# Optimization experiments

Hardware: AMD Instinct MI355X
Metric: run time of the kernel (lower is better)

The kernel has to match this reference:

```python
import jax, jax.numpy as jnp
import numpy as np
from jax import lax

N_PCD, N_RGB = 5000, 15000
C_PCD, C_RGB = 32, 128
N_ANCHOR, SA_RADIUS, SA_NS = 4096, 0.1, 32
NB_RADIUS, NB_K = 0.2, 64


def _fps(xyz, npoint):
    # farthest point sampling, first index = 0 (CUDA convention)
    n = xyz.shape[0]
    def step(carry, _):
        dists, last = carry
        d = jnp.sum((xyz - xyz[last]) ** 2, axis=-1)
        dists = jnp.minimum(dists, d)
        nxt = jnp.argmax(dists).astype(jnp.int32)
        return (dists, nxt), nxt
    init = (jnp.full((n,), 1e10, xyz.dtype), jnp.int32(0))
    _, rest = lax.scan(step, init, None, length=npoint - 1)
    return jnp.concatenate([jnp.zeros((1,), jnp.int32), rest])


def _ball_query(radius, nsample, points, centers):
    # first `nsample` points within radius of each center; pad with first hit
    n = points.shape[0]
    d2 = jnp.sum((centers[:, None, :] - points[None, :, :]) ** 2, axis=-1)  # [M,N]
    key_ = jnp.where(d2 < radius * radius, jnp.arange(n, dtype=jnp.float32), float(n))
    vals, idx = lax.top_k(-key_, nsample)  # smallest in-range indices first
    valid = vals > -(float(n) - 0.5)
    return jnp.where(valid, idx, idx[:, :1])


def _detection_scores(xyz, features):
    # xyz [N,3], features [N,C]
    n = xyz.shape[0]
    nb = _ball_query(NB_RADIUS, NB_K, xyz, xyz)                       # [N,K]
    feats = jnp.concatenate([features, jnp.zeros_like(features[:1])], 0)
    nb = jnp.concatenate([nb, jnp.full((1, NB_K), n, nb.dtype)], 0)   # shadow row
    feats = feats / (jnp.max(feats) + 1e-6)
    nf = feats[nb]                                                    # [N+1,K,C]
    num = jnp.maximum(jnp.sum((nb >= 0).astype(feats.dtype), 1, keepdims=True), 1.0)
    mean = jnp.sum(nf, axis=1) / num
    local_max = jax.nn.softplus(feats - mean)
    dw_max = jnp.max(feats, axis=1, keepdims=True)
    dw_score = feats / (1e-6 + dw_max)
    return jnp.max(local_max * dw_score, axis=1)[:-1]                 # [N]


def setup_inputs() -> dict:
    key = jax.random.key(0)
    ks = jax.random.split(key, 12)
    def w(k, o, i):
        return jax.random.normal(k, (o, i), jnp.float32) * 0.05
    return {
        'pcd_xyz': jax.random.uniform(ks[0], (N_PCD, 3), jnp.float32),
        'pcd_features': jax.random.normal(ks[1], (N_PCD, C_PCD), jnp.float32),
        'rgb_xyz': jax.random.uniform(ks[2], (1, N_RGB, 3), jnp.float32),
        'rgb_features': jax.random.normal(ks[3], (1, C_RGB, N_RGB), jnp.float32),
        'sa_W1': w(ks[4], 128, 3 + C_PCD + C_RGB), 'sa_b1': jnp.zeros((128,), jnp.float32),
        'sa_W2': w(ks[5], 128, 128), 'sa_b2': jnp.zeros((128,), jnp.float32),
        'sa_W3': w(ks[6], 128, 128), 'sa_b3': jnp.zeros((128,), jnp.float32),
        'fp_W1': w(ks[7], 128, C_PCD + C_RGB + 128), 'fp_b1': jnp.zeros((128,), jnp.float32),
        'fp_W2': w(ks[8], 32, 128), 'fp_b2': jnp.zeros((32,), jnp.float32),
    }


def reference(pcd_xyz, pcd_features, rgb_xyz, rgb_features,
              sa_W1, sa_b1, sa_W2, sa_b2, sa_W3, sa_b3,
              fp_W1, fp_b1, fp_W2, fp_b2):
    rgb_xyz = rgb_xyz[0]                       # [N_rgb,3]
    rgb_feat = rgb_features[0].T               # [N_rgb,128]
    # zero-padded modality channels, then concat clouds
    pcd_exp = jnp.concatenate([pcd_features, jnp.zeros((N_PCD, C_RGB), pcd_features.dtype)], 1)
    rgb_exp = jnp.concatenate([jnp.zeros((N_RGB, C_PCD), rgb_feat.dtype), rgb_feat], 1)
    xyz = jnp.concatenate([pcd_xyz, rgb_xyz], 0)      # [N,3]
    feat = jnp.concatenate([pcd_exp, rgb_exp], 0)     # [N,160]

    # --- PointnetSAModuleVotes: FPS + ball query + shared MLP + max pool ---
    fidx = _fps(xyz, N_ANCHOR)
    new_xyz = xyz[fidx]                               # [A,3]
    nb = _ball_query(SA_RADIUS, SA_NS, xyz, new_xyz)  # [A,S]
    gxyz = (xyz[nb] - new_xyz[:, None, :]) / SA_RADIUS  # normalize_xyz
    g = jnp.concatenate([gxyz, feat[nb]], -1)          # [A,S,163]
    h = g
    for W, b in ((sa_W1, sa_b1), (sa_W2, sa_b2), (sa_W3, sa_b3)):
        h = jax.nn.relu(jnp.einsum('asc,oc->aso', h, W) + b)
    sa_feat = jnp.max(h, axis=1)                       # [A,128]

    # --- PointnetFPModule: three-NN inverse-distance interpolation + MLP ---
    d2 = jnp.sum((xyz[:, None, :] - new_xyz[None, :, :]) ** 2, -1)  # [N,A]
    negd, nn_idx = lax.top_k(-d2, 3)
    wgt = 1.0 / (-negd + 1e-8)
    wgt = wgt / jnp.sum(wgt, -1, keepdims=True)
    interp = jnp.einsum('nkc,nk->nc', sa_feat[nn_idx], wgt)         # [N,128]
    f = jnp.concatenate([interp, feat], -1)                         # [N,288]
    f = jax.nn.relu(f @ fp_W1.T + fp_b1)
    f = jax.nn.relu(f @ fp_W2.T + fp_b2)                            # [N,32]

    fp_feat = f[:N_PCD]                                             # [N_pcd,32]
    vote_scores = _detection_scores(pcd_xyz, fp_feat)               # [N_pcd]
    norm = jnp.maximum(jnp.linalg.norm(fp_feat, axis=1, keepdims=True), 1e-12)
    vote_features = fp_feat / norm
    return (pcd_xyz, vote_scores, vote_features)
```

## Files before the change

kernel.cpp:

```cpp
#include <hip/hip_runtime.h>

#define N_ALL 20000
#define NPCD  5000
#define NRGB  15000
#define CPCD  32
#define CRGB  128
#define CF    160
#define NA    4096
#define SANS  32
#define NBK   64
#define K1    163
#define K1P   168
#define HD    128
#define FPK   288
#define NSOA  20480

__global__ void prep_kernel(const float* __restrict__ pcd_xyz,
                            const float* __restrict__ pcd_feat,
                            const float* __restrict__ rgb_xyz,
                            const float* __restrict__ rgb_feat,
                            const float* __restrict__ sa_W1,
                            float* __restrict__ xyz,
                            float* __restrict__ feat,
                            float* __restrict__ W1p) {
  const int TOT = N_ALL*CF + N_ALL*3 + HD*K1P;
  for (int id = blockIdx.x*blockDim.x + threadIdx.x; id < TOT; id += gridDim.x*blockDim.x) {
    if (id < N_ALL*CF) {
      int r = id / CF, c = id - r*CF;
      float v = 0.0f;
      if (r < NPCD) { if (c < CPCD) v = pcd_feat[r*CPCD + c]; }
      else          { if (c >= CPCD) v = rgb_feat[(c - CPCD)*NRGB + (r - NPCD)]; }
      feat[id] = v;
    } else if (id < N_ALL*CF + N_ALL*3) {
      int e = id - N_ALL*CF;
      xyz[e] = (e < NPCD*3) ? pcd_xyz[e] : rgb_xyz[e - NPCD*3];
    } else {
      int e = id - (N_ALL*CF + N_ALL*3);
      int o = e / K1P, c = e - o*K1P;
      W1p[e] = (c < K1) ? sa_W1[o*K1 + c] : 0.0f;
    }
  }
}

static __device__ __forceinline__ unsigned spread4(unsigned v) {
  return (v & 1u) | ((v & 2u) << 2) | ((v & 4u) << 4) | ((v & 8u) << 6);
}
static __device__ __forceinline__ unsigned morton12(float x, float y, float z) {
  int ix = (int)(x * 16.0f); ix = ix < 0 ? 0 : (ix > 15 ? 15 : ix);
  int iy = (int)(y * 16.0f); iy = iy < 0 ? 0 : (iy > 15 ? 15 : iy);
  int iz = (int)(z * 16.0f); iz = iz < 0 ? 0 : (iz > 15 ? 15 : iz);
  return spread4((unsigned)ix) | (spread4((unsigned)iy) << 1) | (spread4((unsigned)iz) << 2);
}

__global__ void __launch_bounds__(1024) sort_kernel(const float* __restrict__ pcd_xyz,
                                                    const float* __restrict__ rgb_xyz,
                                                    float* __restrict__ xsoa,
                                                    float* __restrict__ ysoa,
                                                    float* __restrict__ zsoa,
                                                    unsigned short* __restrict__ orig16) {
  __shared__ unsigned hist[4096];
  __shared__ unsigned ssum[1024];
  const int t = threadIdx.x;
  for (int i = t; i < 4096; i += 1024) hist[i] = 0u;
  __syncthreads();
  for (int p = t; p < N_ALL; p += 1024) {
    float x, y, z;
    if (p < NPCD) { x = pcd_xyz[3*p]; y = pcd_xyz[3*p+1]; z = pcd_xyz[3*p+2]; }
    else { int q = p - NPCD; x = rgb_xyz[3*q]; y = rgb_xyz[3*q+1]; z = rgb_xyz[3*q+2]; }
    atomicAdd(&hist[morton12(x, y, z)], 1u);
  }
  __syncthreads();
  unsigned h0 = hist[4*t], h1 = hist[4*t+1], h2 = hist[4*t+2], h3 = hist[4*t+3];
  unsigned mysum = h0 + h1 + h2 + h3;
  ssum[t] = mysum;
  __syncthreads();
  for (int off = 1; off < 1024; off <<= 1) {
    unsigned add = (t >= off) ? ssum[t - off] : 0u;
    __syncthreads();
    ssum[t] += add;
    __syncthreads();
  }
  unsigned excl = ssum[t] - mysum;
  hist[4*t]   = excl;
  hist[4*t+1] = excl + h0;
  hist[4*t+2] = excl + h0 + h1;
  hist[4*t+3] = excl + h0 + h1 + h2;
  __syncthreads();
  for (int p = t; p < N_ALL; p += 1024) {
    float x, y, z;
    if (p < NPCD) { x = pcd_xyz[3*p]; y = pcd_xyz[3*p+1]; z = pcd_xyz[3*p+2]; }
    else { int q = p - NPCD; x = rgb_xyz[3*q]; y = rgb_xyz[3*q+1]; z = rgb_xyz[3*q+2]; }
    unsigned dst = atomicAdd(&hist[morton12(x, y, z)], 1u);
    xsoa[dst] = x; ysoa[dst] = y; zsoa[dst] = z; orig16[dst] = (unsigned short)p;
  }
  for (int i = N_ALL + t; i < NSOA; i += 1024) {
    xsoa[i] = 0.0f; ysoa[i] = 0.0f; zsoa[i] = 0.0f; orig16[i] = 0;
  }
}

typedef float v2f __attribute__((ext_vector_type(2)));

template <int CTRL>
static __device__ __forceinline__ unsigned dpp_min_u32(unsigned v) {
  int s = __builtin_amdgcn_update_dpp((int)v, (int)v, CTRL, 0xF, 0xF, false);
  unsigned u = (unsigned)s;
  return v < u ? v : u;
}

__global__ void __launch_bounds__(1024)
__attribute__((amdgpu_waves_per_eu(2, 4)))
fps_kernel(const float* __restrict__ xsoa,
           const float* __restrict__ ysoa,
           const float* __restrict__ zsoa,
           const unsigned short* __restrict__ orig16,
           const float* __restrict__ pcd_xyz,
           int* __restrict__ fidx,
           float* __restrict__ axyz) {
  #pragma clang fp contract(off)
  const int t = threadIdx.x;
  const int lane = t & 63;
  __shared__ unsigned long long ls[4];
  if (t < 4) ls[t] = ~0ull;
  const int base = 20 * t;
  v2f X[10], Y[10], Z[10], D[10];
  unsigned idk[20];
  #pragma unroll
  for (int j = 0; j < 10; j++) {
    int p = base + 2*j;
    X[j] = *(const v2f*)(xsoa + p);
    Y[j] = *(const v2f*)(ysoa + p);
    Z[j] = *(const v2f*)(zsoa + p);
    D[j].x = (p     < N_ALL) ? 1e10f : -1.0f;
    D[j].y = (p + 1 < N_ALL) ? 1e10f : -1.0f;
    idk[2*j]   = ((unsigned)orig16[p]     << 15) | (unsigned)p;
    idk[2*j+1] = ((unsigned)orig16[p + 1] << 15) | (unsigned)(p + 1);
  }
  float blx = 1e30f, bhx = -1e30f, bly = 1e30f, bhy = -1e30f, blz = 1e30f, bhz = -1e30f;
  #pragma unroll
  for (int j = 0; j < 10; j++) {
    blx = fminf(blx, fminf(X[j].x, X[j].y)); bhx = fmaxf(bhx, fmaxf(X[j].x, X[j].y));
    bly = fminf(bly, fminf(Y[j].x, Y[j].y)); bhy = fmaxf(bhy, fmaxf(Y[j].x, Y[j].y));
    blz = fminf(blz, fminf(Z[j].x, Z[j].y)); bhz = fmaxf(bhz, fmaxf(Z[j].x, Z[j].y));
  }
  float tmaxc = (base < N_ALL) ? 1e10f : -1.0f;
  unsigned invd = 0xFFFFFFFFu, k32 = 0xFFFFFFFFu;
  float cx = pcd_xyz[0], cy = pcd_xyz[1], cz = pcd_xyz[2];
  if (t == 0) { fidx[0] = 0; axyz[0] = cx; axyz[1] = cy; axyz[2] = cz; }
  __syncthreads();
  for (int it = 1; it < NA; ++it) {
    const int s = it & 3;
    float tdx = fmaxf(fmaxf(blx - cx, cx - bhx), 0.0f);
    float tdy = fmaxf(fmaxf(bly - cy, cy - bhy), 0.0f);
    float tdz = fmaxf(fmaxf(blz - cz, cz - bhz), 0.0f);
    float lb2 = (tdx*tdx + tdy*tdy) + tdz*tdz;
    if (lb2 * 0.99f < tmaxc) {
      v2f cxv = {cx, cx}, cyv = {cy, cy}, czv = {cz, cz};
      float m[10];
      #pragma unroll
      for (int j = 0; j < 10; j++) {
        v2f dx = X[j] - cxv;
        v2f dy = Y[j] - cyv;
        v2f dz = Z[j] - czv;
        v2f d  = (dx*dx + dy*dy) + dz*dz;
        D[j].x = fminf(D[j].x, d.x);
        D[j].y = fminf(D[j].y, d.y);
        m[j] = fmaxf(D[j].x, D[j].y);
      }
      float m0 = fmaxf(m[0], m[1]), m1 = fmaxf(m[2], m[3]);
      float m2 = fmaxf(m[4], m[5]), m3 = fmaxf(m[6], m[7]);
      float tmax = fmaxf(fmaxf(fmaxf(m0, m1), fmaxf(m2, m3)), fmaxf(m[8], m[9]));
      tmaxc = tmax;
      invd = ~__float_as_uint(tmax);
      unsigned kk = 0xFFFFFFFFu;
      #pragma unroll
      for (int j = 0; j < 10; j++) {
        unsigned c0 = (D[j].x == tmax) ? idk[2*j]     : 0xFFFFFFFFu;
        unsigned c1 = (D[j].y == tmax) ? idk[2*j + 1] : 0xFFFFFFFFu;
        unsigned cm = c0 < c1 ? c0 : c1;
        kk = kk < cm ? kk : cm;
      }
      k32 = kk;
    }
    unsigned wi = invd;
    wi = dpp_min_u32<0x111>(wi);
    wi = dpp_min_u32<0x112>(wi);
    wi = dpp_min_u32<0x114>(wi);
    wi = dpp_min_u32<0x118>(wi);
    wi = dpp_min_u32<0x142>(wi);
    wi = dpp_min_u32<0x143>(wi);
    unsigned wmin = (unsigned)__builtin_amdgcn_readlane((int)wi, 63);
    unsigned sel = (invd == wmin) ? k32 : 0xFFFFFFFFu;
    sel = dpp_min_u32<0x111>(sel);
    sel = dpp_min_u32<0x112>(sel);
    sel = dpp_min_u32<0x114>(sel);
    sel = dpp_min_u32<0x118>(sel);
    sel = dpp_min_u32<0x142>(sel);
    sel = dpp_min_u32<0x143>(sel);
    if (lane == 63)
      atomicMin(&ls[s], ((unsigned long long)wmin << 32) | (unsigned long long)sel);
    if (t == 0) ls[(it + 2) & 3] = ~0ull;
    __syncthreads();
    unsigned lo = (unsigned)ls[s];
    unsigned pos = lo & 32767u;
    cx = xsoa[pos]; cy = ysoa[pos]; cz = zsoa[pos];
    if (t == 0) {
      fidx[it] = (int)(lo >> 15);
      axyz[3*it] = cx; axyz[3*it+1] = cy; axyz[3*it+2] = cz;
    }
  }
}

__global__ void sa_bq_kernel(const float* __restrict__ xyz,
                             const float* __restrict__ axyz,
                             int* __restrict__ nb) {
  #pragma clang fp contract(off)
  int wv = threadIdx.x >> 6, lane = threadIdx.x & 63;
  int a = blockIdx.x*4 + wv;
  float ax = axyz[3*a], ay = axyz[3*a+1], az = axyz[3*a+2];
  int cnt = 0, my = 0;
  for (int base = 0; base < N_ALL; base += 64) {
    int p = base + lane;
    bool in = false;
    if (p < N_ALL) {
      float dx = ax - xyz[3*p], dy = ay - xyz[3*p+1], dz = az - xyz[3*p+2];
      float d2 = (dx*dx + dy*dy) + dz*dz;
      in = d2 < 0.01f;
    }
    unsigned long long mask = __ballot(in);
    while (mask && cnt < SANS) {
      int b = __builtin_ctzll(mask);
      mask &= mask - 1;
      if (cnt == lane) my = base + b;
      cnt++;
    }
    if (cnt >= SANS) break;
  }
  int f0 = __shfl(my, 0);
  if (lane < SANS) nb[a*SANS + lane] = (lane < cnt) ? my : f0;
}

__global__ void det_bq_kernel(const float* __restrict__ pxyz,
                              int* __restrict__ nb) {
  #pragma clang fp contract(off)
  int wv = threadIdx.x >> 6, lane = threadIdx.x & 63;
  int i = blockIdx.x*4 + wv;
  float ax = pxyz[3*i], ay = pxyz[3*i+1], az = pxyz[3*i+2];
  int cnt = 0, my = 0;
  for (int base = 0; base < NPCD; base += 64) {
    int p = base + lane;
    bool in = false;
    if (p < NPCD) {
      float dx = ax - pxyz[3*p], dy = ay - pxyz[3*p+1], dz = az - pxyz[3*p+2];
      float d2 = (dx*dx + dy*dy) + dz*dz;
      in = d2 < 0.04f;
    }
    unsigned long long mask = __ballot(in);
    while (mask && cnt < NBK) {
      int b = __builtin_ctzll(mask);
      mask &= mask - 1;
      if (cnt == lane) my = base + b;
      cnt++;
    }
    if (cnt >= NBK) break;
  }
  int f0 = __shfl(my, 0);
  nb[i*NBK + lane] = (lane < cnt) ? my : f0;
}

__global__ void __launch_bounds__(128) sa_mlp_kernel(const float* __restrict__ xyz,
                                                     const float* __restrict__ feat,
                                                     const float* __restrict__ axyz,
                                                     const int* __restrict__ nb,
                                                     const float* __restrict__ W1p,
                                                     const float* __restrict__ b1,
                                                     const float* __restrict__ W2,
                                                     const float* __restrict__ b2,
                                                     const float* __restrict__ W3,
                                                     const float* __restrict__ b3,
                                                     float* __restrict__ sa_feat) {
  __shared__ float g[SANS*K1P];
  __shared__ float h1[SANS*HD];
  __shared__ int nbs[SANS];
  int a = blockIdx.x, tid = threadIdx.x;
  if (tid < SANS) nbs[tid] = nb[a*SANS + tid];
  float ax = axyz[3*a], ay = axyz[3*a+1], az = axyz[3*a+2];
  __syncthreads();
  for (int e = tid; e < SANS*K1P; e += 128) {
    int s = e / K1P, c = e - s*K1P;
    float v = 0.0f;
    int p = nbs[s];
    if (c < 3) {
      float pc  = xyz[3*p + c];
      float acx = (c == 0) ? ax : ((c == 1) ? ay : az);
      v = (pc - acx) / 0.1f;
    } else if (c < K1) {
      v = feat[p*CF + (c - 3)];
    }
    g[e] = v;
  }
  __syncthreads();
  const int o = tid;
  float acc[SANS];
  #pragma unroll
  for (int s = 0; s < SANS; s++) acc[s] = b1[o];
  for (int kc = 0; kc < 21; kc++) {
    const float4* wp = (const float4*)(W1p + o*K1P + kc*8);
    float4 w0 = wp[0], w1 = wp[1];
    #pragma unroll
    for (int s = 0; s < SANS; s++) {
      const float4* gp = (const float4*)(g + s*K1P + kc*8);
      float4 g0 = gp[0], g1 = gp[1];
      acc[s] += w0.x*g0.x + w0.y*g0.y + w0.z*g0.z + w0.w*g0.w
              + w1.x*g1.x + w1.y*g1.y + w1.z*g1.z + w1.w*g1.w;
    }
  }
  #pragma unroll
  for (int s = 0; s < SANS; s++) h1[s*HD + o] = fmaxf(acc[s], 0.0f);
  __syncthreads();
  #pragma unroll
  for (int s = 0; s < SANS; s++) acc[s] = b2[o];
  for (int kc = 0; kc < 16; kc++) {
    const float4* wp = (const float4*)(W2 + o*HD + kc*8);
    float4 w0 = wp[0], w1 = wp[1];
    #pragma unroll
    for (int s = 0; s < SANS; s++) {
      const float4* gp = (const float4*)(h1 + s*HD + kc*8);
      float4 g0 = gp[0], g1 = gp[1];
      acc[s] += w0.x*g0.x + w0.y*g0.y + w0.z*g0.z + w0.w*g0.w
              + w1.x*g1.x + w1.y*g1.y + w1.z*g1.z + w1.w*g1.w;
    }
  }
  float* h2 = g;
  #pragma unroll
  for (int s = 0; s < SANS; s++) h2[s*HD + o] = fmaxf(acc[s], 0.0f);
  __syncthreads();
  #pragma unroll
  for (int s = 0; s < SANS; s++) acc[s] = b3[o];
  for (int kc = 0; kc < 16; kc++) {
    const float4* wp = (const float4*)(W3 + o*HD + kc*8);
    float4 w0 = wp[0], w1 = wp[1];
    #pragma unroll
    for (int s = 0; s < SANS; s++) {
      const float4* gp = (const float4*)(h2 + s*HD + kc*8);
      float4 g0 = gp[0], g1 = gp[1];
      acc[s] += w0.x*g0.x + w0.y*g0.y + w0.z*g0.z + w0.w*g0.w
              + w1.x*g1.x + w1.y*g1.y + w1.z*g1.z + w1.w*g1.w;
    }
  }
  float m = 0.0f;
  #pragma unroll
  for (int s = 0; s < SANS; s++) m = fmaxf(m, fmaxf(acc[s], 0.0f));
  sa_feat[a*HD + o] = m;
}

#define INSERT3(v) { if ((v) < t0){ t2=t1; t1=t0; t0=(v);} \
                     else if ((v) < t1){ t2=t1; t1=(v);} \
                     else if ((v) < t2){ t2=(v);} }

__global__ void nn_interp_kernel(const float* __restrict__ xyz,
                                 const float* __restrict__ feat,
                                 const float* __restrict__ axyz,
                                 const float* __restrict__ sa_feat,
                                 float* __restrict__ F) {
  #pragma clang fp contract(off)
  int wv = threadIdx.x >> 6, lane = threadIdx.x & 63;
  int p = blockIdx.x*4 + wv;
  float px = xyz[3*p], py = xyz[3*p+1], pz = xyz[3*p+2];
  unsigned long long t0 = ~0ull, t1 = ~0ull, t2 = ~0ull;
  for (int j = 0; j < 64; j++) {
    int a = lane + (j << 6);
    float dx = px - axyz[3*a], dy = py - axyz[3*a+1], dz = pz - axyz[3*a+2];
    float d2 = (dx*dx + dy*dy) + dz*dz;
    unsigned long long pk = ((unsigned long long)__float_as_uint(d2) << 32) | (unsigned)a;
    INSERT3(pk);
  }
  #pragma unroll
  for (int off = 1; off < 64; off <<= 1) {
    unsigned long long b0 = __shfl_xor(t0, off);
    unsigned long long b1 = __shfl_xor(t1, off);
    unsigned long long b2 = __shfl_xor(t2, off);
    INSERT3(b0); INSERT3(b1); INSERT3(b2);
  }
  float d0 = __uint_as_float((unsigned)(t0 >> 32));
  float d1 = __uint_as_float((unsigned)(t1 >> 32));
  float d2v = __uint_as_float((unsigned)(t2 >> 32));
  int a0 = (int)(t0 & 0xFFFFFFFFull), a1 = (int)(t1 & 0xFFFFFFFFull), a2 = (int)(t2 & 0xFFFFFFFFull);
  float w0 = 1.0f/(d0 + 1e-8f), w1 = 1.0f/(d1 + 1e-8f), w2 = 1.0f/(d2v + 1e-8f);
  float wsum = w0 + w1 + w2;
  w0 /= wsum; w1 /= wsum; w2 /= wsum;
  const float* s0 = sa_feat + a0*HD;
  const float* s1 = sa_feat + a1*HD;
  const float* s2 = sa_feat + a2*HD;
  float* Fr = F + p*FPK;
  Fr[lane]      = w0*s0[lane]    + w1*s1[lane]    + w2*s2[lane];
  Fr[lane + 64] = w0*s0[lane+64] + w1*s1[lane+64] + w2*s2[lane+64];
  const float* fr = feat + p*CF;
  Fr[HD + lane]      = fr[lane];
  Fr[HD + lane + 64] = fr[lane + 64];
  if (lane < 32) Fr[HD + 128 + lane] = fr[128 + lane];
}

__global__ void __launch_bounds__(128) fp1_kernel(const float* __restrict__ F,
                                                  const float* __restrict__ W,
                                                  const float* __restrict__ b,
                                                  float* __restrict__ H) {
  __shared__ float A[32*FPK];
  int base = blockIdx.x*32, tid = threadIdx.x;
  for (int e = tid; e < 32*FPK; e += 128) {
    int r = e / FPK; int gr = base + r;
    A[e] = (gr < NPCD) ? F[gr*FPK + (e - r*FPK)] : 0.0f;
  }
  __syncthreads();
  const int o = tid;
  float acc[32];
  #pragma unroll
  for (int r = 0; r < 32; r++) acc[r] = b[o];
  for (int kc = 0; kc < 36; kc++) {
    const float4* wp = (const float4*)(W + o*FPK + kc*8);
    float4 w0 = wp[0], w1 = wp[1];
    #pragma unroll
    for (int r = 0; r < 32; r++) {
      const float4* ap = (const float4*)(A + r*FPK + kc*8);
      float4 a0 = ap[0], a1 = ap[1];
      acc[r] += w0.x*a0.x + w0.y*a0.y + w0.z*a0.z + w0.w*a0.w
              + w1.x*a1.x + w1.y*a1.y + w1.z*a1.z + w1.w*a1.w;
    }
  }
  #pragma unroll
  for (int r = 0; r < 32; r++) {
    int gr = base + r;
    if (gr < NPCD) H[gr*HD + o] = fmaxf(acc[r], 0.0f);
  }
}

__global__ void __launch_bounds__(256) fp2_kernel(const float* __restrict__ Hin,
                                                  const float* __restrict__ W,
                                                  const float* __restrict__ b,
                                                  float* __restrict__ fpf,
                                                  unsigned* __restrict__ gmax) {
  if (blockIdx.x == 0 && threadIdx.x == 0) *gmax = 0u;
  __shared__ float A[32*HD];
  int base = blockIdx.x*32, tid = threadIdx.x;
  for (int e = tid; e < 32*HD; e += 256) {
    int r = e >> 7; int gr = base + r;
    A[e] = (gr < NPCD) ? Hin[gr*HD + (e & 127)] : 0.0f;
  }
  __syncthreads();
  int o = tid & 31, rg = tid >> 5;
  float acc[4];
  #pragma unroll
  for (int j = 0; j < 4; j++) acc[j] = b[o];
  for (int kc = 0; kc < 16; kc++) {
    const float4* wp = (const float4*)(W + o*HD + kc*8);
    float4 w0 = wp[0], w1 = wp[1];
    #pragma unroll
    for (int j = 0; j < 4; j++) {
      int r = rg + (j << 3);
      const float4* ap = (const float4*)(A + r*HD + kc*8);
      float4 a0 = ap[0], a1 = ap[1];
      acc[j] += w0.x*a0.x + w0.y*a0.y + w0.z*a0.z + w0.w*a0.w
              + w1.x*a1.x + w1.y*a1.y + w1.z*a1.z + w1.w*a1.w;
    }
  }
  #pragma unroll
  for (int j = 0; j < 4; j++) {
    int gr = base + rg + (j << 3);
    if (gr < NPCD) fpf[gr*CPCD + o] = fmaxf(acc[j], 0.0f);
  }
}

__global__ void gmax_kernel(const float* __restrict__ fpf, unsigned* __restrict__ gmax) {
  int id = blockIdx.x*256 + threadIdx.x;
  float m = (id < NPCD*CPCD) ? fpf[id] : 0.0f;
  #pragma unroll
  for (int off = 1; off < 64; off <<= 1) m = fmaxf(m, __shfl_xor(m, off));
  if ((threadIdx.x & 63) == 0) atomicMax(gmax, __float_as_uint(m));
}

__global__ void det_score_kernel(const float* __restrict__ fpf,
                                 const int* __restrict__ nbd,
                                 const unsigned* __restrict__ gmax,
                                 float* __restrict__ outs) {
  int wv = threadIdx.x >> 6, lane = threadIdx.x & 63;
  int i = blockIdx.x*4 + wv;
  float g = __uint_as_float(*gmax);
  float scale = 1.0f / (g + 1e-6f);
  int c = lane & 31, h = lane >> 5;
  float sum = 0.0f;
  const int* nbr = nbd + i*NBK + h*32;
  for (int k = 0; k < 32; k++) {
    int idx = nbr[k];
    sum += fpf[idx*CPCD + c];
  }
  sum += __shfl_xor(sum, 32);
  float mean = (sum * scale) * 0.015625f;
  float fi = fpf[i*CPCD + c] * scale;
  float x = fi - mean;
  float lm = fmaxf(x, 0.0f) + log1pf(expf(-fabsf(x)));
  float dm = fi;
  #pragma unroll
  for (int off = 1; off < 64; off <<= 1) dm = fmaxf(dm, __shfl_xor(dm, off));
  float dw = fi / (1e-6f + dm);
  float pr = lm * dw;
  #pragma unroll
  for (int off = 1; off < 64; off <<= 1) pr = fmaxf(pr, __shfl_xor(pr, off));
  if (lane == 0) outs[i] = pr;
}

__global__ void vote_out_kernel(const float* __restrict__ pcd_xyz,
                                const float* __restrict__ fpf,
                                float* __restrict__ dout) {
  int id = blockIdx.x*256 + threadIdx.x;
  if (id < NPCD*3) dout[id] = pcd_xyz[id];
  int r = id - NPCD*3;
  if (r >= 0 && r < NPCD) {
    float ss = 0.0f;
    const float* fr = fpf + r*CPCD;
    #pragma unroll
    for (int cc = 0; cc < CPCD; cc++) ss += fr[cc]*fr[cc];
    float nrm = fmaxf(sqrtf(ss), 1e-12f);
    float* vf = dout + NPCD*3 + NPCD + r*CPCD;
    #pragma unroll
    for (int cc = 0; cc < CPCD; cc++) vf[cc] = fr[cc] / nrm;
  }
}

extern "C" void kernel_launch(void* const* d_in, const int* in_sizes, int n_in,
                              void* d_out, int out_size, void* d_ws, size_t ws_size,
                              hipStream_t stream) {
  const float* pcd_xyz      = (const float*)d_in[0];
  const float* pcd_features = (const float*)d_in[1];
  const float* rgb_xyz      = (const float*)d_in[2];
  const float* rgb_features = (const float*)d_in[3];
  const float* sa_W1 = (const float*)d_in[4];
  const float* sa_b1 = (const float*)d_in[5];
  const float* sa_W2 = (const float*)d_in[6];
  const float* sa_b2 = (const float*)d_in[7];
  const float* sa_W3 = (const float*)d_in[8];
  const float* sa_b3 = (const float*)d_in[9];
  const float* fp_W1 = (const float*)d_in[10];
  const float* fp_b1 = (const float*)d_in[11];
  const float* fp_W2 = (const float*)d_in[12];
  const float* fp_b2 = (const float*)d_in[13];
  float* out = (float*)d_out;

  float* xyz  = (float*)d_ws;
  float* feat = xyz  + 60000;
  float* W1p  = feat + 3200000;
  float* axyz = W1p  + 21504;
  float* saf  = axyz + 12288;
  float* F    = saf  + 524288;
  float* Hb   = F    + 1440000;
  float* fpf  = Hb   + 640000;
  int*   fidx = (int*)(fpf + 160000);
  int*   nbsa = fidx + 4096;
  int*   nbdet= nbsa + 131072;
  unsigned* gmaxp = (unsigned*)(nbdet + 320000);
  float* xsoa = (float*)(gmaxp + 1);
  float* ysoa = xsoa + NSOA;
  float* zsoa = ysoa + NSOA;
  unsigned short* orig16 = (unsigned short*)(zsoa + NSOA);

  prep_kernel<<<2048, 256, 0, stream>>>(pcd_xyz, pcd_features, rgb_xyz, rgb_features,
                                        sa_W1, xyz, feat, W1p);
  sort_kernel<<<1, 1024, 0, stream>>>(pcd_xyz, rgb_xyz, xsoa, ysoa, zsoa, orig16);
  fps_kernel<<<1, 1024, 0, stream>>>(xsoa, ysoa, zsoa, orig16, pcd_xyz, fidx, axyz);
  sa_bq_kernel<<<1024, 256, 0, stream>>>(xyz, axyz, nbsa);
  sa_mlp_kernel<<<4096, 128, 0, stream>>>(xyz, feat, axyz, nbsa, W1p, sa_b1,
                                          sa_W2, sa_b2, sa_W3, sa_b3, saf);
  nn_interp_kernel<<<1250, 256, 0, stream>>>(xyz, feat, axyz, saf, F);
  fp1_kernel<<<157, 128, 0, stream>>>(F, fp_W1, fp_b1, Hb);
  fp2_kernel<<<157, 256, 0, stream>>>(Hb, fp_W2, fp_b2, fpf, gmaxp);
  det_bq_kernel<<<1250, 256, 0, stream>>>(pcd_xyz, nbdet);
  gmax_kernel<<<625, 256, 0, stream>>>(fpf, gmaxp);
  det_score_kernel<<<1250, 256, 0, stream>>>(fpf, nbdet, gmaxp, out + NPCD*3);
  vote_out_kernel<<<79, 256, 0, stream>>>(pcd_xyz, fpf, out);
}
```

Baseline: 5.425 ms.

## Overlap detection ball query with FPS blocks and replace atomicMin with per-wave slots

The detection ball query moves into extra blocks of the single-block FPS launch, so it runs on otherwise idle CUs while the serial FPS loop executes, and its separate launch is removed. Inside FPS, the per-iteration shared atomicMin and slot reset are replaced by each wave writing its packed key to a double-buffered per-wave slot, and every thread then reduces the 16 keys after the barrier. This drops the initial barrier and the atomic work from the FPS critical path, but adds 16 LDS reads and a min tree per iteration on every thread.

```diff
diff --git a/kernel.cpp b/kernel.cpp
--- a/kernel.cpp
+++ b/kernel.cpp
@@ -106,6 +106,10 @@
   unsigned u = (unsigned)s;
   return v < u ? v : u;
 }
+static __device__ __forceinline__ unsigned long long u64min(unsigned long long a,
+                                                           unsigned long long b) {
+  return a < b ? a : b;
+}
 
 __global__ void __launch_bounds__(1024)
 __attribute__((amdgpu_waves_per_eu(2, 4)))
@@ -115,12 +119,43 @@
            const unsigned short* __restrict__ orig16,
            const float* __restrict__ pcd_xyz,
            int* __restrict__ fidx,
-           float* __restrict__ axyz) {
+           float* __restrict__ axyz,
+           int* __restrict__ nbdet) {
   #pragma clang fp contract(off)
   const int t = threadIdx.x;
-  const int lane = t & 63;
-  __shared__ unsigned long long ls[4];
-  if (t < 4) ls[t] = ~0ull;
+  const int lane = t & 63, wv = t >> 6;
+
+  if (blockIdx.x > 0) {
+    int b = (int)blockIdx.x - 1;
+    for (int e = 0; e < 2; e++) {
+      int i = b*32 + wv*2 + e;
+      if (i >= NPCD) break;
+      float ax = pcd_xyz[3*i], ay = pcd_xyz[3*i+1], az = pcd_xyz[3*i+2];
+      int cnt = 0, my = 0;
+      for (int bb = 0; bb < NPCD; bb += 64) {
+        int p = bb + lane;
+        bool in = false;
+        if (p < NPCD) {
+          float dx = ax - pcd_xyz[3*p], dy = ay - pcd_xyz[3*p+1], dz = az - pcd_xyz[3*p+2];
+          float d2 = (dx*dx + dy*dy) + dz*dz;
+          in = d2 < 0.04f;
+        }
+        unsigned long long mask = __ballot(in);
+        while (mask && cnt < NBK) {
+          int bit = __builtin_ctzll(mask);
+          mask &= mask - 1;
+          if (cnt == lane) my = bb + bit;
+          cnt++;
+        }
+        if (cnt >= NBK) break;
+      }
+      int f0 = __shfl(my, 0);
+      nbdet[i*NBK + lane] = (lane < cnt) ? my : f0;
+    }
+    return;
+  }
+
+  __shared__ unsigned long long lsw[2][16];
   const int base = 20 * t;
   v2f X[10], Y[10], Z[10], D[10];
   unsigned idk[20];
@@ -146,9 +181,8 @@
   unsigned invd = 0xFFFFFFFFu, k32 = 0xFFFFFFFFu;
   float cx = pcd_xyz[0], cy = pcd_xyz[1], cz = pcd_xyz[2];
   if (t == 0) { fidx[0] = 0; axyz[0] = cx; axyz[1] = cy; axyz[2] = cz; }
-  __syncthreads();
   for (int it = 1; it < NA; ++it) {
-    const int s = it & 3;
+    const int par = it & 1;
     float tdx = fmaxf(fmaxf(blx - cx, cx - bhx), 0.0f);
     float tdy = fmaxf(fmaxf(bly - cy, cy - bhy), 0.0f);
     float tdz = fmaxf(fmaxf(blz - cz, cz - bhz), 0.0f);
@@ -197,10 +231,19 @@
     sel = dpp_min_u32<0x142>(sel);
     sel = dpp_min_u32<0x143>(sel);
     if (lane == 63)
-      atomicMin(&ls[s], ((unsigned long long)wmin << 32) | (unsigned long long)sel);
-    if (t == 0) ls[(it + 2) & 3] = ~0ull;
+      lsw[par][wv] = ((unsigned long long)wmin << 32) | (unsigned long long)sel;
     __syncthreads();
-    unsigned lo = (unsigned)ls[s];
+    unsigned long long k0 = u64min(lsw[par][0],  lsw[par][1]);
+    unsigned long long k1 = u64min(lsw[par][2],  lsw[par][3]);
+    unsigned long long k2 = u64min(lsw[par][4],  lsw[par][5]);
+    unsigned long long k3 = u64min(lsw[par][6],  lsw[par][7]);
+    unsigned long long k4 = u64min(lsw[par][8],  lsw[par][9]);
+    unsigned long long k5 = u64min(lsw[par][10], lsw[par][11]);
+    unsigned long long k6 = u64min(lsw[par][12], lsw[par][13]);
+    unsigned long long k7 = u64min(lsw[par][14], lsw[par][15]);
+    unsigned long long kmin = u64min(u64min(u64min(k0, k1), u64min(k2, k3)),
+                                     u64min(u64min(k4, k5), u64min(k6, k7)));
+    unsigned lo = (unsigned)kmin;
     unsigned pos = lo & 32767u;
     cx = xsoa[pos]; cy = ysoa[pos]; cz = zsoa[pos];
     if (t == 0) {
@@ -237,34 +280,6 @@
   }
   int f0 = __shfl(my, 0);
   if (lane < SANS) nb[a*SANS + lane] = (lane < cnt) ? my : f0;
-}
-
-__global__ void det_bq_kernel(const float* __restrict__ pxyz,
-                              int* __restrict__ nb) {
-  #pragma clang fp contract(off)
-  int wv = threadIdx.x >> 6, lane = threadIdx.x & 63;
-  int i = blockIdx.x*4 + wv;
-  float ax = pxyz[3*i], ay = pxyz[3*i+1], az = pxyz[3*i+2];
-  int cnt = 0, my = 0;
-  for (int base = 0; base < NPCD; base += 64) {
-    int p = base + lane;
-    bool in = false;
-    if (p < NPCD) {
-      float dx = ax - pxyz[3*p], dy = ay - pxyz[3*p+1], dz = az - pxyz[3*p+2];
-      float d2 = (dx*dx + dy*dy) + dz*dz;
-      in = d2 < 0.04f;
-    }
-    unsigned long long mask = __ballot(in);
-    while (mask && cnt < NBK) {
-      int b = __builtin_ctzll(mask);
-      mask &= mask - 1;
-      if (cnt == lane) my = base + b;
-      cnt++;
-    }
-    if (cnt >= NBK) break;
-  }
-  int f0 = __shfl(my, 0);
-  nb[i*NBK + lane] = (lane < cnt) ? my : f0;
 }
 
 __global__ void __launch_bounds__(128) sa_mlp_kernel(const float* __restrict__ xyz,
@@ -564,14 +579,13 @@
   prep_kernel<<<2048, 256, 0, stream>>>(pcd_xyz, pcd_features, rgb_xyz, rgb_features,
                                         sa_W1, xyz, feat, W1p);
   sort_kernel<<<1, 1024, 0, stream>>>(pcd_xyz, rgb_xyz, xsoa, ysoa, zsoa, orig16);
-  fps_kernel<<<1, 1024, 0, stream>>>(xsoa, ysoa, zsoa, orig16, pcd_xyz, fidx, axyz);
+  fps_kernel<<<158, 1024, 0, stream>>>(xsoa, ysoa, zsoa, orig16, pcd_xyz, fidx, axyz, nbdet);
   sa_bq_kernel<<<1024, 256, 0, stream>>>(xyz, axyz, nbsa);
   sa_mlp_kernel<<<4096, 128, 0, stream>>>(xyz, feat, axyz, nbsa, W1p, sa_b1,
                                           sa_W2, sa_b2, sa_W3, sa_b3, saf);
   nn_interp_kernel<<<1250, 256, 0, stream>>>(xyz, feat, axyz, saf, F);
   fp1_kernel<<<157, 128, 0, stream>>>(F, fp_W1, fp_b1, Hb);
   fp2_kernel<<<157, 256, 0, stream>>>(Hb, fp_W2, fp_b2, fpf, gmaxp);
-  det_bq_kernel<<<1250, 256, 0, stream>>>(pcd_xyz, nbdet);
   gmax_kernel<<<625, 256, 0, stream>>>(fpf, gmaxp);
   det_score_kernel<<<1250, 256, 0, stream>>>(fpf, nbdet, gmaxp, out + NPCD*3);
   vote_out_kernel<<<79, 256, 0, stream>>>(pcd_xyz, fpf, out);
```

Result: slower. 6.057 ms (+11.6%).
